# Kernel tuning notes

Measured on AMD Instinct MI355X. Metric: run time of the kernel, lower is better.

## Reference

```python
import jax, jax.numpy as jnp
import numpy as np

B, HN, N1, N2, S = 32, 12, 256, 320, 256  # S = hardcoded 256 buffer size
EPS = 1e-5


def setup_inputs() -> dict:
    key = jax.random.key(0)
    ks = jax.random.split(key, 6)
    attn_rgb = jax.random.normal(ks[0], (B, HN, N1, N2), dtype=jnp.float32)
    attn_tir = jax.random.normal(ks[1], (B, HN, N1, N2), dtype=jnp.float32)
    # per-batch unique indices in [0, 256): permutation (collision-free scatter)
    perm = jax.vmap(lambda k: jax.random.permutation(k, S))(jax.random.split(ks[2], B))
    global_index_s = perm[:, :N1].astype(jnp.int32)
    # LayerNorm(512) params
    ln_g = jnp.ones((2 * S,), jnp.float32)
    ln_b = jnp.zeros((2 * S,), jnp.float32)
    # Linear(512,256) xavier-uniform weight, zero bias (stored as [in,out])
    lim1 = float(np.sqrt(6.0 / (2 * S + S)))
    W1 = jax.random.uniform(ks[3], (2 * S, S), jnp.float32, -lim1, lim1)
    b1 = jnp.zeros((S,), jnp.float32)
    # Linear(256,512)
    lim2 = float(np.sqrt(6.0 / (S + 2 * S)))
    W2 = jax.random.uniform(ks[4], (S, 2 * S), jnp.float32, -lim2, lim2)
    b2 = jnp.zeros((2 * S,), jnp.float32)
    return {"attn_rgb": attn_rgb, "attn_tir": attn_tir, "global_index_s": global_index_s,
            "ln_g": ln_g, "ln_b": ln_b, "W1": W1, "b1": b1, "W2": W2, "b2": b2}


def reference(attn_rgb, attn_tir, global_index_s, ln_g, ln_b, W1, b1, W2, b2):
    Bv, hn, n1, _ = attn_rgb.shape
    idx = jnp.broadcast_to(global_index_s[:, None, :].astype(jnp.int32), (Bv, hn, n1))  # [B,hn,N1]
    # detach() in torch source -> stop_gradient on the max-pooled path
    mx_rgb = jax.lax.stop_gradient(attn_rgb).max(-1)  # [B,hn,N1]
    mx_tir = jax.lax.stop_gradient(attn_tir).max(-1)
    bi = jnp.arange(Bv)[:, None, None]
    hi = jnp.arange(hn)[None, :, None]
    vex_rgb = jnp.zeros((Bv, hn, S), attn_rgb.dtype).at[bi, hi, idx].set(mx_rgb)
    vex_tir = jnp.zeros((Bv, hn, S), attn_tir.dtype).at[bi, hi, idx].set(mx_tir)
    v = jnp.concatenate([vex_rgb, vex_tir], axis=-1)  # [B,hn,512]
    # LayerNorm(512)
    mu = v.mean(-1, keepdims=True)
    var = v.var(-1, keepdims=True)
    v = (v - mu) * jax.lax.rsqrt(var + EPS) * ln_g + ln_b
    # SE MLP: Linear -> ReLU -> Linear -> Sigmoid
    h = jax.nn.relu(jnp.einsum('bhe,ef->bhf', v, W1) + b1)
    g = jax.nn.sigmoid(jnp.einsum('bhf,fe->bhe', h, W2) + b2)  # [B,hn,512]
    # gather gates back via indices and modulate
    g_rgb = jnp.take_along_axis(g[..., :S], idx, axis=-1)[..., None]  # [B,hn,N1,1]
    g_tir = jnp.take_along_axis(g[..., S:], idx, axis=-1)[..., None]
    attn_rgb_col = g_rgb * attn_rgb
    attn_tir_col = g_tir * attn_tir
    return (attn_tir_col, attn_rgb_col)
```

## Files before the change

### kernel.cpp

```cpp
#include <hip/hip_runtime.h>
#include <hip/hip_bf16.h>
#include <math.h>

#define BB   32
#define HN   12
#define N1   256
#define N2   320
#define SS   256
#define BH   (BB*HN)
#define R4   (N2/4)
#define SLICE4 ((size_t)N1*R4)

typedef float v4f __attribute__((ext_vector_type(4)));

__global__ __launch_bounds__(256, 2) void k_fused(
    const float* __restrict__ rgb, const float* __restrict__ tir,
    const int*   __restrict__ gidx,
    const float* __restrict__ ln_g, const float* __restrict__ ln_b,
    const float* __restrict__ W1,  const float* __restrict__ b1,
    const float* __restrict__ W2,  const float* __restrict__ b2,
    v4f* __restrict__ outTir, v4f* __restrict__ outRgb)
{
    __shared__ float mxs[2 * SS];
    __shared__ float v[2 * SS];
    __shared__ float hs[SS];
    __shared__ float gs[2 * SS];
    __shared__ float growR[SS];
    __shared__ float growT[SS];
    __shared__ int   sidx_s[SS];
    __shared__ float red[8];

    const int bh   = (int)blockIdx.x;
    const int b    = bh / HN;
    const int t    = (int)threadIdx.x;
    const int w    = t >> 6;
    const int lane = t & 63;

    sidx_s[t] = gidx[b * SS + t];
    v[t] = 0.f; v[t + SS] = 0.f;

    const v4f* srcR = (const v4f*)rgb + (size_t)bh * SLICE4;
    const v4f* srcT = (const v4f*)tir + (size_t)bh * SLICE4;

    for (int rr = 0; rr < 64; rr += 4) {
        const int r = w * 64 + rr;
        v4f aR[4], bRv[4], aT[4], bTv[4];
#pragma unroll
        for (int q = 0; q < 4; ++q) {
            const v4f* pR = srcR + (size_t)(r + q) * R4;
            const v4f* pT = srcT + (size_t)(r + q) * R4;
            aR[q]  = pR[lane];
            bRv[q] = pR[64 + (lane & 15)];
            aT[q]  = pT[lane];
            bTv[q] = pT[64 + (lane & 15)];
        }
#pragma unroll
        for (int q = 0; q < 4; ++q) {
            float mR = fmaxf(fmaxf(fmaxf(aR[q].x, aR[q].y), fmaxf(aR[q].z, aR[q].w)),
                             fmaxf(fmaxf(bRv[q].x, bRv[q].y), fmaxf(bRv[q].z, bRv[q].w)));
            float mT = fmaxf(fmaxf(fmaxf(aT[q].x, aT[q].y), fmaxf(aT[q].z, aT[q].w)),
                             fmaxf(fmaxf(bTv[q].x, bTv[q].y), fmaxf(bTv[q].z, bTv[q].w)));
#pragma unroll
            for (int off = 32; off; off >>= 1) {
                mR = fmaxf(mR, __shfl_xor(mR, off));
                mT = fmaxf(mT, __shfl_xor(mT, off));
            }
            if (lane == 0) { mxs[r + q] = mR; mxs[SS + r + q] = mT; }
        }
    }
    __syncthreads();

    {
        int sidx = sidx_s[t];
        v[sidx]      = mxs[t];
        v[sidx + SS] = mxs[SS + t];
    }
    __syncthreads();

    {
        float x0 = v[t], x1 = v[t + SS];
        float s  = x0 + x1;
        float sq = x0 * x0 + x1 * x1;
#pragma unroll
        for (int off = 32; off; off >>= 1) {
            s  += __shfl_xor(s, off);
            sq += __shfl_xor(sq, off);
        }
        if (lane == 0) { red[w] = s; red[4 + w] = sq; }
        __syncthreads();
        s  = red[0] + red[1] + red[2] + red[3];
        sq = red[4] + red[5] + red[6] + red[7];
        const float mu   = s * (1.f / 512.f);
        const float var  = sq * (1.f / 512.f) - mu * mu;
        const float rstd = rsqrtf(var + 1e-5f);
        v[t]      = (x0 - mu) * rstd * ln_g[t]      + ln_b[t];
        v[t + SS] = (x1 - mu) * rstd * ln_g[t + SS] + ln_b[t + SS];
    }
    __syncthreads();

    {
        float a0 = b1[t], a1 = 0.f;
#pragma unroll 8
        for (int e = 0; e < SS; ++e)       a0 = fmaf(v[e], W1[e * SS + t], a0);
#pragma unroll 8
        for (int e = SS; e < 2 * SS; ++e)  a1 = fmaf(v[e], W1[e * SS + t], a1);
        hs[t] = fmaxf(a0 + a1, 0.f);
    }
    __syncthreads();

    {
        float lo0 = b2[t], lo1 = 0.f, hi0 = b2[t + SS], hi1 = 0.f;
#pragma unroll 8
        for (int f = 0; f < 128; ++f) {
            float hv = hs[f];
            lo0 = fmaf(hv, W2[f * 2 * SS + t],      lo0);
            hi0 = fmaf(hv, W2[f * 2 * SS + t + SS], hi0);
        }
#pragma unroll 8
        for (int f = 128; f < SS; ++f) {
            float hv = hs[f];
            lo1 = fmaf(hv, W2[f * 2 * SS + t],      lo1);
            hi1 = fmaf(hv, W2[f * 2 * SS + t + SS], hi1);
        }
        gs[t]      = 1.f / (1.f + expf(-(lo0 + lo1)));
        gs[t + SS] = 1.f / (1.f + expf(-(hi0 + hi1)));
    }
    __syncthreads();

    growR[t] = gs[sidx_s[t]];
    growT[t] = gs[sidx_s[t] + SS];
    __syncthreads();

    {
        v4f* dstR = outRgb + (size_t)bh * SLICE4;
        v4f* dstT = outTir + (size_t)bh * SLICE4;
        for (int k = 0; k < 80; k += 8) {
            v4f aR[8], aT[8];
#pragma unroll
            for (int q = 0; q < 8; ++q) {
                unsigned i = (unsigned)(k + q) * 256u + (unsigned)t;
                aR[q] = srcR[i];
                aT[q] = srcT[i];
            }
#pragma unroll
            for (int q = 0; q < 8; ++q) {
                unsigned i   = (unsigned)(k + q) * 256u + (unsigned)t;
                unsigned row = i / 80u;
                v4f oR = aR[q] * growR[row];
                v4f oT = aT[q] * growT[row];
                __builtin_nontemporal_store(oT, dstT + i);
                __builtin_nontemporal_store(oR, dstR + i);
            }
        }
    }
}

extern "C" void kernel_launch(void* const* d_in, const int* in_sizes, int n_in,
                              void* d_out, int out_size, void* d_ws, size_t ws_size,
                              hipStream_t stream)
{
    const float* attn_rgb = (const float*)d_in[0];
    const float* attn_tir = (const float*)d_in[1];
    const int*   gidx     = (const int*)  d_in[2];
    const float* ln_g     = (const float*)d_in[3];
    const float* ln_b     = (const float*)d_in[4];
    const float* W1       = (const float*)d_in[5];
    const float* b1       = (const float*)d_in[6];
    const float* W2       = (const float*)d_in[7];
    const float* b2       = (const float*)d_in[8];

    v4f* outTir = (v4f*)d_out;
    v4f* outRgb = outTir + (size_t)BH * SLICE4;

    k_fused<<<BH, 256, 0, stream>>>(attn_rgb, attn_tir, gidx, ln_g, ln_b,
                                    W1, b1, W2, b2, outTir, outRgb);
}
```

Measured before the change: 138.9 us.

## Split each (b,h) slice across two blocks with redundant gate computation

Launches two blocks per (batch, head) slice. Each block still computes the full row maxima, LayerNorm and SE MLP redundantly, then modulates and writes only half of the rows. The two blocks read the rows in opposite orders so that their reads overlap in cache. This doubles the grid to 768 blocks and raises the occupancy hint to improve latency hiding across the CUs. In exchange the max-reduction reads and the MLP weight traffic are duplicated.

```diff
diff --git a/kernel.cpp b/kernel.cpp
--- a/kernel.cpp
+++ b/kernel.cpp
@@ -1,5 +1,4 @@
 #include <hip/hip_runtime.h>
-#include <hip/hip_bf16.h>
 #include <math.h>
 
 #define BB   32
@@ -13,7 +12,7 @@
 
 typedef float v4f __attribute__((ext_vector_type(4)));
 
-__global__ __launch_bounds__(256, 2) void k_fused(
+__global__ __launch_bounds__(256, 3) void k_pair(
     const float* __restrict__ rgb, const float* __restrict__ tir,
     const int*   __restrict__ gidx,
     const float* __restrict__ ln_g, const float* __restrict__ ln_b,
@@ -25,12 +24,14 @@
     __shared__ float v[2 * SS];
     __shared__ float hs[SS];
     __shared__ float gs[2 * SS];
-    __shared__ float growR[SS];
-    __shared__ float growT[SS];
     __shared__ int   sidx_s[SS];
     __shared__ float red[8];
+    __shared__ float growR[128];
+    __shared__ float growT[128];
 
-    const int bh   = (int)blockIdx.x;
+    const int j    = (int)blockIdx.x;
+    const int bh   = j >> 1;
+    const int half = j & 1;
     const int b    = bh / HN;
     const int t    = (int)threadIdx.x;
     const int w    = t >> 6;
@@ -39,33 +40,30 @@
     sidx_s[t] = gidx[b * SS + t];
     v[t] = 0.f; v[t + SS] = 0.f;
 
-    const v4f* srcR = (const v4f*)rgb + (size_t)bh * SLICE4;
-    const v4f* srcT = (const v4f*)tir + (size_t)bh * SLICE4;
+    const float* sliceR = rgb + (size_t)bh * (N1 * N2);
+    const float* sliceT = tir + (size_t)bh * (N1 * N2);
 
-    for (int rr = 0; rr < 64; rr += 4) {
-        const int r = w * 64 + rr;
-        v4f aR[4], bRv[4], aT[4], bTv[4];
+    for (int uu = 0; uu < 128; uu += 8) {
+        v4f a[8], b8[8];
 #pragma unroll
-        for (int q = 0; q < 4; ++q) {
-            const v4f* pR = srcR + (size_t)(r + q) * R4;
-            const v4f* pT = srcT + (size_t)(r + q) * R4;
-            aR[q]  = pR[lane];
-            bRv[q] = pR[64 + (lane & 15)];
-            aT[q]  = pT[lane];
-            bTv[q] = pT[64 + (lane & 15)];
+        for (int q = 0; q < 8; ++q) {
+            int lin = w * 128 + uu + q;
+            int u   = half ? 511 - lin : lin;
+            const v4f* p = (const v4f*)((u >= SS ? sliceT : sliceR)
+                                        + (size_t)(u & 255) * N2);
+            a[q]  = p[lane];
+            b8[q] = p[64 + (lane & 15)];
         }
 #pragma unroll
-        for (int q = 0; q < 4; ++q) {
-            float mR = fmaxf(fmaxf(fmaxf(aR[q].x, aR[q].y), fmaxf(aR[q].z, aR[q].w)),
-                             fmaxf(fmaxf(bRv[q].x, bRv[q].y), fmaxf(bRv[q].z, bRv[q].w)));
-            float mT = fmaxf(fmaxf(fmaxf(aT[q].x, aT[q].y), fmaxf(aT[q].z, aT[q].w)),
-                             fmaxf(fmaxf(bTv[q].x, bTv[q].y), fmaxf(bTv[q].z, bTv[q].w)));
+        for (int q = 0; q < 8; ++q) {
+            float m = fmaxf(fmaxf(fmaxf(a[q].x, a[q].y), fmaxf(a[q].z, a[q].w)),
+                            fmaxf(fmaxf(b8[q].x, b8[q].y), fmaxf(b8[q].z, b8[q].w)));
 #pragma unroll
-            for (int off = 32; off; off >>= 1) {
-                mR = fmaxf(mR, __shfl_xor(mR, off));
-                mT = fmaxf(mT, __shfl_xor(mT, off));
+            for (int off = 32; off; off >>= 1) m = fmaxf(m, __shfl_xor(m, off));
+            if (lane == 0) {
+                int lin = w * 128 + uu + q;
+                mxs[half ? 511 - lin : lin] = m;
             }
-            if (lane == 0) { mxs[r + q] = mR; mxs[SS + r + q] = mT; }
         }
     }
     __syncthreads();
@@ -127,29 +125,36 @@
     }
     __syncthreads();
 
-    growR[t] = gs[sidx_s[t]];
-    growT[t] = gs[sidx_s[t] + SS];
+    if (t < 128) {
+        int s = sidx_s[half * 128 + t];
+        growR[t] = gs[s];
+        growT[t] = gs[s + SS];
+    }
     __syncthreads();
 
     {
-        v4f* dstR = outRgb + (size_t)bh * SLICE4;
-        v4f* dstT = outTir + (size_t)bh * SLICE4;
+        const v4f* sR4 = (const v4f*)sliceR;
+        const v4f* sT4 = (const v4f*)sliceT;
+        v4f* dR = outRgb + (size_t)bh * SLICE4;
+        v4f* dT = outTir + (size_t)bh * SLICE4;
+        const unsigned base = (unsigned)(half * 128) * 80u;
         for (int k = 0; k < 80; k += 8) {
-            v4f aR[8], aT[8];
+            v4f a[8]; float g[8];
 #pragma unroll
             for (int q = 0; q < 8; ++q) {
-                unsigned i = (unsigned)(k + q) * 256u + (unsigned)t;
-                aR[q] = srcR[i];
-                aT[q] = srcT[i];
+                unsigned i  = (unsigned)(k + q) * 256u + (unsigned)t;
+                int isRgb   = i >= 10240u;
+                unsigned jj = isRgb ? i - 10240u : i;
+                a[q] = (isRgb ? sR4 : sT4)[base + jj];
+                g[q] = (isRgb ? growR : growT)[jj / 80u];
             }
 #pragma unroll
             for (int q = 0; q < 8; ++q) {
-                unsigned i   = (unsigned)(k + q) * 256u + (unsigned)t;
-                unsigned row = i / 80u;
-                v4f oR = aR[q] * growR[row];
-                v4f oT = aT[q] * growT[row];
-                __builtin_nontemporal_store(oT, dstT + i);
-                __builtin_nontemporal_store(oR, dstR + i);
+                unsigned i  = (unsigned)(k + q) * 256u + (unsigned)t;
+                int isRgb   = i >= 10240u;
+                unsigned jj = isRgb ? i - 10240u : i;
+                __builtin_nontemporal_store(a[q] * g[q],
+                                            (isRgb ? dR : dT) + base + jj);
             }
         }
     }
@@ -172,6 +177,6 @@
     v4f* outTir = (v4f*)d_out;
     v4f* outRgb = outTir + (size_t)BH * SLICE4;
 
-    k_fused<<<BH, 256, 0, stream>>>(attn_rgb, attn_tir, gidx, ln_g, ln_b,
-                                    W1, b1, W2, b2, outTir, outRgb);
+    k_pair<<<2 * BH, 256, 0, stream>>>(attn_rgb, attn_tir, gidx, ln_g, ln_b,
+                                       W1, b1, W2, b2, outTir, outRgb);
 }
```

New measurement: 172.5 us. +24.2%, slower.
